# Optimization experiments

Measured on AMD Instinct MI355X. Metric: run time of the kernel, lower is better.

Reference implementation:

```python
import jax, jax.numpy as jnp
import numpy as np

B, H, S, D = 4, 16, 2048, 64
SCALE = 8.0  # sqrt(D)
NEG = -1000000000.0


def setup_inputs() -> dict:
    key = jax.random.key(0)
    kq, kk, kv = jax.random.split(key, 3)
    q = jax.random.normal(kq, (B, H, S, D), dtype=jnp.float32)
    k = jax.random.normal(kk, (B, H, S, D), dtype=jnp.float32)
    v = jax.random.normal(kv, (B, H, S, D), dtype=jnp.float32)
    # causal mask: True means masked out (matches torch masked_fill)
    mask = jnp.triu(jnp.ones((S, S), dtype=bool), k=1)[None, None, :, :]
    mask = jnp.broadcast_to(mask, (B, 1, S, S))
    return {"q": q, "k": k, "v": v, "mask": mask}


def reference(q, k, v, mask):
    # score = q @ k^T / scale  -> [B,H,S,S]
    score = jnp.einsum("bhqd,bhkd->bhqk", q, k) / SCALE
    score = jnp.where(mask, NEG, score)
    probs = jax.nn.softmax(score, axis=-1)
    context = jnp.einsum("bhqk,bhkd->bhqd", probs, v)
    return context
```

## Files before the change

kernel.cpp:

```cpp
#include <hip/hip_runtime.h>

#define SQ 2048
#define DH 64
#define BK 64
#define NQT 32
#define NBH 64
#define M0 8.0f

#define WS_BYTES ((size_t)2 * NBH * SQ * DH * 2)

typedef float f32x4 __attribute__((ext_vector_type(4)));
typedef __bf16 bf16x8 __attribute__((ext_vector_type(8)));
typedef _Float16 f16x4 __attribute__((ext_vector_type(4)));
typedef _Float16 f16x8 __attribute__((ext_vector_type(8)));
typedef __fp16 fp16x2 __attribute__((ext_vector_type(2)));
typedef unsigned short u16x8 __attribute__((ext_vector_type(8)));
typedef unsigned int u32x4 __attribute__((ext_vector_type(4)));

#define WAIT_VM(N) asm volatile("s_waitcnt vmcnt(" #N ")" ::: "memory")

static __device__ __forceinline__ unsigned int pkbf(float a, float b) {
#if __has_builtin(__builtin_amdgcn_cvt_pk_bf16_f32)
  typedef __bf16 bf16x2 __attribute__((ext_vector_type(2)));
  bf16x2 r = __builtin_amdgcn_cvt_pk_bf16_f32(a, b);
  return __builtin_bit_cast(unsigned int, r);
#else
  unsigned int ua = __builtin_bit_cast(unsigned int, a);
  unsigned int ub = __builtin_bit_cast(unsigned int, b);
  ua += 0x7fffu + ((ua >> 16) & 1u);
  ub += 0x7fffu + ((ub >> 16) & 1u);
  return (ua >> 16) | (ub & 0xffff0000u);
#endif
}

static __device__ __forceinline__ unsigned int pkf16(float a, float b) {
  fp16x2 r = __builtin_amdgcn_cvt_pkrtz(a, b);
  return __builtin_bit_cast(unsigned int, r);
}

static __device__ __forceinline__ f32x4 mfma_qk(u16x8 a, u16x8 b, f32x4 c) {
  return __builtin_amdgcn_mfma_f32_16x16x32_bf16(
      __builtin_bit_cast(bf16x8, a), __builtin_bit_cast(bf16x8, b), c, 0, 0, 0);
}

static __device__ __forceinline__ f32x4 mfma_pv(f16x4 a, f16x4 b, f32x4 c) {
  return __builtin_amdgcn_mfma_f32_16x16x16f16(a, b, c, 0, 0, 0);
}

static __device__ __forceinline__ f32x4 mfma_pv32(f16x8 a, f16x8 b, f32x4 c) {
  return __builtin_amdgcn_mfma_f32_16x16x32_f16(a, b, c, 0, 0, 0);
}

static __device__ __forceinline__ void ld16(unsigned short* l, const unsigned short* g) {
  __builtin_amdgcn_global_load_lds(
      (const __attribute__((address_space(1))) unsigned int*)(const void*)g,
      (__attribute__((address_space(3))) unsigned int*)(void*)l, 16, 0, 0);
}

static __device__ __forceinline__ void store_tile(float* wb, float* dst,
                                                  const f32x4* o, int lane,
                                                  int l15, int quad) {
#pragma unroll
  for (int dt = 0; dt < 4; ++dt) {
    const int colw = dt * 16 + quad * 4;
    *(f32x4*)&wb[l15 * 64 + (colw ^ ((l15 & 3) * 16))] = o[dt];
  }
  __builtin_amdgcn_wave_barrier();
#pragma unroll
  for (int j = 0; j < 4; ++j) {
    const int row = j * 4 + (lane >> 4);
    const int colw = (lane & 15) * 4;
    f32x4 v = *(const f32x4*)&wb[row * 64 + (colw ^ ((row & 3) * 16))];
    *(f32x4*)&dst[row * 64 + colw] = v;
  }
}

__global__ __launch_bounds__(256) void prep(const float* __restrict__ K,
                                            const float* __restrict__ V,
                                            unsigned short* __restrict__ Kf,
                                            unsigned short* __restrict__ Vf) {
  const int bh = (int)blockIdx.x >> 5;
  const int st = (int)blockIdx.x & 31;
  const int tid = threadIdx.x;
  __shared__ __align__(16) unsigned short T[DH * 64];
  {
    const int kvb = (tid >> 4) * 4, vdb = (tid & 15) * 4;
    const float* vp = V + ((size_t)bh * SQ + st * 64 + kvb) * DH + vdb;
    f32x4 r0 = *(const f32x4*)vp, r1 = *(const f32x4*)(vp + DH),
          r2 = *(const f32x4*)(vp + 2 * DH), r3 = *(const f32x4*)(vp + 3 * DH);
    const int uu = kvb >> 3, h = (kvb >> 2) & 1;
#pragma unroll
    for (int i = 0; i < 4; ++i) {
      const int d = vdb + i;
      uint2 w = {pkf16(r0[i], r1[i]), pkf16(r2[i], r3[i])};
      *(uint2*)&T[d * 64 + ((uu ^ (d & 7)) * 8) + h * 4] = w;
    }
  }
  {
    const size_t kin = ((size_t)bh * SQ + st * 64) * DH;
    unsigned short* kfo = Kf + (size_t)bh * SQ * DH + (size_t)st * 64 * DH;
#pragma unroll
    for (int e = 0; e < 2; ++e) {
      const int L = tid * 2 + e;
      const int l15 = L & 15, quad = (L >> 4) & 3, c = (L >> 6) & 1, nt = (L >> 7) & 3;
      const int krow = (nt >> 1) * 32 + ((l15 >> 2) & 3) * 8 + (nt & 1) * 4 + (l15 & 3);
      const float* kp = K + kin + (size_t)krow * DH + (c * 4 + quad) * 8;
      f32x4 x = *(const f32x4*)kp, y = *(const f32x4*)(kp + 4);
      u32x4 w = {pkbf(x[0], x[1]), pkbf(x[2], x[3]), pkbf(y[0], y[1]), pkbf(y[2], y[3])};
      *(u32x4*)&kfo[L * 8] = w;
    }
  }
  __syncthreads();
  {
    unsigned short* vfo = Vf + (size_t)bh * SQ * DH + (size_t)st * 64 * DH;
#pragma unroll
    for (int e = 0; e < 2; ++e) {
      const int L = tid * 2 + e;
      const int l15 = L & 15, quad = (L >> 4) & 3, dt = (L >> 6) & 3, n2 = (L >> 8) & 1;
      const int d = dt * 16 + l15, uu = n2 * 4 + quad;
      u16x8 val = *(const u16x8*)&T[d * 64 + ((uu ^ (d & 7)) * 8)];
      *(u16x8*)&vfo[L * 8] = val;
    }
  }
}

__global__ __launch_bounds__(512, 4) void fa_main(
    const float* __restrict__ Q, const unsigned short* __restrict__ Kf,
    const unsigned short* __restrict__ Vf, float* __restrict__ O) {
  const int lin = (int)blockIdx.x;
  const int xcd = lin & 7, u = lin >> 3;
  const int hh = u & 7;
  const int p = (int)((0x32104567u >> ((u >> 3) * 4)) & 15u);
  const int bh = hh * 8 + xcd;
  const int tend = 4 * p + 3;

  const int tid = threadIdx.x;
  const int wv = tid >> 6;
  const int lane = tid & 63;
  const int l15 = lane & 15;
  const int quad = lane >> 4;

  __shared__ __align__(16) unsigned short SS[4][8192];

  const size_t hq = (size_t)bh * (SQ * DH);
  const unsigned short* KfH = Kf + (size_t)bh * SQ * DH;
  const unsigned short* VfH = Vf + (size_t)bh * SQ * DH;

  const int qbase = p * 256 + wv * 32;
  const int dtw = 4 * p + (wv >> 1);
  const int qo = (wv & 1) * 32;

  u16x8 qf[2][2];
  {
    const float scq = 0.125f * 1.4426950408889634f;
#pragma unroll
    for (int f = 0; f < 2; ++f) {
      const float* qp = Q + hq + (size_t)(qbase + 16 * f + l15) * DH + quad * 8;
#pragma unroll
      for (int c = 0; c < 2; ++c) {
        f32x4 x = *(const f32x4*)(qp + c * 32);
        f32x4 y = *(const f32x4*)(qp + c * 32 + 4);
        u32x4 w = {pkbf(x[0] * scq, x[1] * scq), pkbf(x[2] * scq, x[3] * scq),
                   pkbf(y[0] * scq, y[1] * scq), pkbf(y[2] * scq, y[3] * scq)};
        qf[f][c] = __builtin_bit_cast(u16x8, w);
      }
    }
  }

  f32x4 o0[4], o1[4], la0, la1;
#pragma unroll
  for (int dt = 0; dt < 4; ++dt) {
    o0[dt] = (f32x4){0.f, 0.f, 0.f, 0.f};
    o1[dt] = (f32x4){0.f, 0.f, 0.f, 0.f};
  }
  la0 = (f32x4){0.f, 0.f, 0.f, 0.f};
  la1 = (f32x4){0.f, 0.f, 0.f, 0.f};
  const f16x8 ones8 = {(_Float16)1.f, (_Float16)1.f, (_Float16)1.f, (_Float16)1.f,
                       (_Float16)1.f, (_Float16)1.f, (_Float16)1.f, (_Float16)1.f};

  auto stage = [&](unsigned short* W, int t) {
#pragma unroll
    for (int j = 0; j < 2; ++j) {
      const int off = wv * 1024 + j * 512 + lane * 8;
      const unsigned short* src = (off < 4096)
                                      ? &KfH[(size_t)t * 4096 + off]
                                      : &VfH[(size_t)t * 4096 + (off - 4096)];
      ld16(&W[off], src);
    }
  };

  auto attend = [&](const unsigned short* B, bool diag) {
    const unsigned short* Ks = B;
    const unsigned short* Vs = B + 4096;
    f32x4 s0[4], s1[4];
#pragma unroll
    for (int nt = 0; nt < 4; ++nt) {
      f32x4 a0 = {-M0, -M0, -M0, -M0}, a1 = {-M0, -M0, -M0, -M0};
#pragma unroll
      for (int c = 0; c < 2; ++c) {
        u16x8 kf = *(const u16x8*)&Ks[(nt * 2 + c) * 512 + lane * 8];
        a0 = mfma_qk(kf, qf[0][c], a0);
        a1 = mfma_qk(kf, qf[1][c], a1);
      }
      s0[nt] = a0;
      s1[nt] = a1;
    }
    if (diag) {
#pragma unroll
      for (int nt = 0; nt < 4; ++nt)
#pragma unroll
        for (int r = 0; r < 4; ++r) {
          const int kvl = (nt >> 1) * 32 + quad * 8 + (nt & 1) * 4 + r;
          if (kvl > qo + l15) s0[nt][r] = -1e30f;
          if (kvl > qo + 16 + l15) s1[nt][r] = -1e30f;
        }
    }
    f16x8 pf0[2], pf1[2];
#pragma unroll
    for (int n2 = 0; n2 < 2; ++n2) {
      f32x4 pe0, po0, pe1, po1;
#pragma unroll
      for (int r = 0; r < 4; ++r) {
        pe0[r] = __builtin_amdgcn_exp2f(s0[2 * n2][r]);
        po0[r] = __builtin_amdgcn_exp2f(s0[2 * n2 + 1][r]);
        pe1[r] = __builtin_amdgcn_exp2f(s1[2 * n2][r]);
        po1[r] = __builtin_amdgcn_exp2f(s1[2 * n2 + 1][r]);
      }
      u32x4 w0 = {pkf16(pe0[0], pe0[1]), pkf16(pe0[2], pe0[3]),
                  pkf16(po0[0], po0[1]), pkf16(po0[2], po0[3])};
      u32x4 w1 = {pkf16(pe1[0], pe1[1]), pkf16(pe1[2], pe1[3]),
                  pkf16(po1[0], po1[1]), pkf16(po1[2], po1[3])};
      pf0[n2] = __builtin_bit_cast(f16x8, w0);
      pf1[n2] = __builtin_bit_cast(f16x8, w1);
    }
#pragma unroll
    for (int n2 = 0; n2 < 2; ++n2) {
      la0 = mfma_pv32(ones8, pf0[n2], la0);
      la1 = mfma_pv32(ones8, pf1[n2], la1);
    }
#pragma unroll
    for (int dt = 0; dt < 4; ++dt) {
#pragma unroll
      for (int n2 = 0; n2 < 2; ++n2) {
        f16x8 vf = *(const f16x8*)&Vs[(n2 * 4 + dt) * 512 + lane * 8];
        o0[dt] = mfma_pv32(vf, pf0[n2], o0[dt]);
        o1[dt] = mfma_pv32(vf, pf1[n2], o1[dt]);
      }
    }
  };

  stage(SS[0], 0);
  stage(SS[1], 1);
  stage(SS[2], 2);
  WAIT_VM(4);
  __builtin_amdgcn_s_barrier();
  __builtin_amdgcn_sched_barrier(0);

  for (int t = 0; t <= tend; ++t) {
    if (t + 3 <= tend) stage(SS[(t + 3) & 3], t + 3);
    if (t <= dtw) attend(SS[t & 3], t == dtw);
    const int rem = tend - t;
    if (rem >= 3) {
      WAIT_VM(4);
    } else if (rem == 2) {
      WAIT_VM(2);
    } else {
      WAIT_VM(0);
    }
    __builtin_amdgcn_s_barrier();
    __builtin_amdgcn_sched_barrier(0);
  }

  float* wb = (float*)SS + wv * 1024;
  {
    const float inv = 1.0f / la0[0];
    f32x4 on[4];
#pragma unroll
    for (int dt = 0; dt < 4; ++dt) on[dt] = o0[dt] * inv;
    store_tile(wb, O + hq + (size_t)(qbase)*DH, on, lane, l15, quad);
  }
  {
    const float inv = 1.0f / la1[0];
    f32x4 on[4];
#pragma unroll
    for (int dt = 0; dt < 4; ++dt) on[dt] = o1[dt] * inv;
    store_tile(wb, O + hq + (size_t)(qbase + 16) * DH, on, lane, l15, quad);
  }
}

__global__ __launch_bounds__(256, 4) void fa_full(
    const float* __restrict__ Q, const float* __restrict__ K,
    const float* __restrict__ V, float* __restrict__ O) {
  const int lin = (int)blockIdx.x;
  const int xcd = lin & 7;
  const int u = lin >> 3;
  const int hh = u & 7;
  const int p = u >> 3;
  const int bh = hh * 8 + xcd;
  const int tid = threadIdx.x;
  const int wv = tid >> 6;
  const int lane = tid & 63;
  const int l15 = lane & 15;
  const int quad = lane >> 4;
  __shared__ __align__(16) unsigned short SMEM[2][2 * BK * DH];
  const size_t hbase = (size_t)bh * (SQ * DH);
  const int krr = tid >> 3, kcc = (tid & 7) * 8;
  const int kvb = (tid >> 4) * 4, vdb = (tid & 15) * 4;
#pragma unroll
  for (int ph = 0; ph < 2; ++ph) {
    const int qt = ph ? (NQT - 1 - p) : p;
    const int wq0 = qt * 64 + wv * 16;
    u16x8 qf[2];
    {
      const float scq = 0.125f * 1.4426950408889634f;
      const float* qp = Q + hbase + (size_t)(wq0 + l15) * DH + quad * 8;
#pragma unroll
      for (int c = 0; c < 2; ++c) {
        f32x4 x = *(const f32x4*)(qp + c * 32);
        f32x4 y = *(const f32x4*)(qp + c * 32 + 4);
        u32x4 w = {pkbf(x[0] * scq, x[1] * scq), pkbf(x[2] * scq, x[3] * scq),
                   pkbf(y[0] * scq, y[1] * scq), pkbf(y[2] * scq, y[3] * scq)};
        qf[c] = __builtin_bit_cast(u16x8, w);
      }
    }
    f32x4 o[4];
#pragma unroll
    for (int dt = 0; dt < 4; ++dt) o[dt] = (f32x4){0.f, 0.f, 0.f, 0.f};
    float l = 0.f;
    f32x4 ka[2][2], va[4];
    {
      const float* kp = K + hbase + (size_t)krr * DH + kcc;
      ka[0][0] = *(const f32x4*)kp;             ka[0][1] = *(const f32x4*)(kp + 4);
      ka[1][0] = *(const f32x4*)(kp + 32 * DH); ka[1][1] = *(const f32x4*)(kp + 32 * DH + 4);
      const float* vp = V + hbase + (size_t)kvb * DH + vdb;
      va[0] = *(const f32x4*)vp;            va[1] = *(const f32x4*)(vp + DH);
      va[2] = *(const f32x4*)(vp + 2 * DH); va[3] = *(const f32x4*)(vp + 3 * DH);
    }
    __syncthreads();
    {
      unsigned short* Ksn = SMEM[0];
      unsigned short* Vsn = SMEM[0] + BK * DH;
#pragma unroll
      for (int h = 0; h < 2; ++h) {
        const int rr = h * 32 + krr;
        u32x4 w = {pkbf(ka[h][0][0], ka[h][0][1]), pkbf(ka[h][0][2], ka[h][0][3]),
                   pkbf(ka[h][1][0], ka[h][1][1]), pkbf(ka[h][1][2], ka[h][1][3])};
        *(u32x4*)&Ksn[rr * DH + (kcc ^ ((rr & 7) * 8))] = w;
      }
#pragma unroll
      for (int i = 0; i < 4; ++i) {
        const int d = vdb + i;
        uint2 w = {pkf16(va[0][i], va[1][i]), pkf16(va[2][i], va[3][i])};
        *(uint2*)&Vsn[d * BK + (kvb ^ ((d & 15) * 4))] = w;
      }
    }
    __syncthreads();
    for (int t = 0; t <= qt; ++t) {
      const unsigned short* Ks = SMEM[t & 1];
      const unsigned short* Vs = SMEM[t & 1] + BK * DH;
      if (t < qt) {
        const int kb2 = (t + 1) * BK;
        const float* kp = K + hbase + (size_t)(kb2 + krr) * DH + kcc;
        ka[0][0] = *(const f32x4*)kp;             ka[0][1] = *(const f32x4*)(kp + 4);
        ka[1][0] = *(const f32x4*)(kp + 32 * DH); ka[1][1] = *(const f32x4*)(kp + 32 * DH + 4);
        const float* vp = V + hbase + (size_t)(kb2 + kvb) * DH + vdb;
        va[0] = *(const f32x4*)vp;            va[1] = *(const f32x4*)(vp + DH);
        va[2] = *(const f32x4*)(vp + 2 * DH); va[3] = *(const f32x4*)(vp + 3 * DH);
      }
      f32x4 s[4];
#pragma unroll
      for (int nt = 0; nt < 4; ++nt) {
        f32x4 acc = {-M0, -M0, -M0, -M0};
#pragma unroll
        for (int c = 0; c < 2; ++c) {
          const int row = nt * 16 + l15;
          u16x8 kf = *(const u16x8*)&Ks[row * DH + ((c * 32 + quad * 8) ^ ((l15 & 7) * 8))];
          acc = mfma_qk(kf, qf[c], acc);
        }
        s[nt] = acc;
      }
      if (t == qt) {
#pragma unroll
        for (int nt = 0; nt < 4; ++nt)
#pragma unroll
          for (int r = 0; r < 4; ++r)
            if (nt * 16 + quad * 4 + r > wv * 16 + l15) s[nt][r] = -1e30f;
      }
      f16x4 pf[4];
#pragma unroll
      for (int nt = 0; nt < 4; ++nt) {
        f32x4 pr;
#pragma unroll
        for (int r = 0; r < 4; ++r) { pr[r] = __builtin_amdgcn_exp2f(s[nt][r]); l += pr[r]; }
        uint2 w2 = {pkf16(pr[0], pr[1]), pkf16(pr[2], pr[3])};
        pf[nt] = __builtin_bit_cast(f16x4, w2);
      }
#pragma unroll
      for (int dt = 0; dt < 4; ++dt) {
        const int d = dt * 16 + l15;
#pragma unroll
        for (int nt = 0; nt < 4; ++nt) {
          f16x4 vf = *(const f16x4*)&Vs[d * BK + ((nt * 16 + quad * 4) ^ (l15 * 4))];
          o[dt] = mfma_pv(vf, pf[nt], o[dt]);
        }
      }
      if (t < qt) {
        unsigned short* Ksn = SMEM[(t + 1) & 1];
        unsigned short* Vsn = SMEM[(t + 1) & 1] + BK * DH;
#pragma unroll
        for (int h = 0; h < 2; ++h) {
          const int rr = h * 32 + krr;
          u32x4 w = {pkbf(ka[h][0][0], ka[h][0][1]), pkbf(ka[h][0][2], ka[h][0][3]),
                     pkbf(ka[h][1][0], ka[h][1][1]), pkbf(ka[h][1][2], ka[h][1][3])};
          *(u32x4*)&Ksn[rr * DH + (kcc ^ ((rr & 7) * 8))] = w;
        }
#pragma unroll
        for (int i = 0; i < 4; ++i) {
          const int d = vdb + i;
          uint2 w = {pkf16(va[0][i], va[1][i]), pkf16(va[2][i], va[3][i])};
          *(uint2*)&Vsn[d * BK + (kvb ^ ((d & 15) * 4))] = w;
        }
        __syncthreads();
      }
    }
    l += __shfl_xor(l, 16, 64);
    l += __shfl_xor(l, 32, 64);
    const float inv = 1.0f / l;
    f32x4 on[4];
#pragma unroll
    for (int dt = 0; dt < 4; ++dt) on[dt] = o[dt] * inv;
    float* wb = (float*)SMEM[(qt + 1) & 1] + wv * 1024;
    store_tile(wb, O + hbase + (size_t)wq0 * DH, on, lane, l15, quad);
  }
}

extern "C" void kernel_launch(void* const* d_in, const int* in_sizes, int n_in,
                              void* d_out, int out_size, void* d_ws, size_t ws_size,
                              hipStream_t stream) {
  const float* q = (const float*)d_in[0];
  const float* k = (const float*)d_in[1];
  const float* v = (const float*)d_in[2];
  float* o = (float*)d_out;
  if (ws_size >= WS_BYTES) {
    unsigned short* Kf = (unsigned short*)d_ws;
    unsigned short* Vf = Kf + (size_t)NBH * SQ * DH;
    prep<<<dim3(NBH * 32), 256, 0, stream>>>(k, v, Kf, Vf);
    fa_main<<<dim3(512), 512, 0, stream>>>(q, Kf, Vf, o);
  } else {
    fa_full<<<dim3(1024), 256, 0, stream>>>(q, k, v, o);
  }
}
```

Measured before the change: 204.0 us.

## Pair complementary causal query tiles per block to balance work in one launch

Each block now processes two query tiles, p and 7-p, back to back, so every block streams the same 36 key/value tiles and causal work is balanced. The grid is halved to 256 blocks and launch bounds drop to 2 waves per SIMD. The pipeline now stages two tiles per step and waits for all loads (vmcnt 0) before each barrier. Output stores go directly to global memory instead of through the LDS-staged store_tile. The risks are lower parallelism with only 256 blocks on a 256-CU device, a pipeline that drains fully every step, and less coalesced output writes.

New measurement: 211.2 us. 3.5% more time.

```diff
diff --git a/kernel.cpp b/kernel.cpp
--- a/kernel.cpp
+++ b/kernel.cpp
@@ -17,7 +17,7 @@
 typedef unsigned short u16x8 __attribute__((ext_vector_type(8)));
 typedef unsigned int u32x4 __attribute__((ext_vector_type(4)));
 
-#define WAIT_VM(N) asm volatile("s_waitcnt vmcnt(" #N ")" ::: "memory")
+#define WAIT_VM0() asm volatile("s_waitcnt vmcnt(0)" ::: "memory")
 
 static __device__ __forceinline__ unsigned int pkbf(float a, float b) {
 #if __has_builtin(__builtin_amdgcn_cvt_pk_bf16_f32)
@@ -124,15 +124,17 @@
   }
 }
 
-__global__ __launch_bounds__(512, 4) void fa_main(
+__global__ __launch_bounds__(512, 2) void fa_main(
     const float* __restrict__ Q, const unsigned short* __restrict__ Kf,
     const unsigned short* __restrict__ Vf, float* __restrict__ O) {
   const int lin = (int)blockIdx.x;
   const int xcd = lin & 7, u = lin >> 3;
   const int hh = u & 7;
-  const int p = (int)((0x32104567u >> ((u >> 3) * 4)) & 15u);
+  const int p = u >> 3;
   const int bh = hh * 8 + xcd;
-  const int tend = 4 * p + 3;
+
+  const int LA = 4 * p + 4;
+  const int NS = 36;
 
   const int tid = threadIdx.x;
   const int wv = tid >> 6;
@@ -146,16 +148,18 @@
   const unsigned short* KfH = Kf + (size_t)bh * SQ * DH;
   const unsigned short* VfH = Vf + (size_t)bh * SQ * DH;
 
-  const int qbase = p * 256 + wv * 32;
-  const int dtw = 4 * p + (wv >> 1);
   const int qo = (wv & 1) * 32;
+  const int qbA = p * 256 + wv * 32;
+  const int qbB = (7 - p) * 256 + wv * 32;
+  const int dtwA = 4 * p + (wv >> 1);
+  const int dtwB = 4 * (7 - p) + (wv >> 1);
 
   u16x8 qf[2][2];
-  {
+  auto loadQ = [&](int qb) {
     const float scq = 0.125f * 1.4426950408889634f;
 #pragma unroll
     for (int f = 0; f < 2; ++f) {
-      const float* qp = Q + hq + (size_t)(qbase + 16 * f + l15) * DH + quad * 8;
+      const float* qp = Q + hq + (size_t)(qb + 16 * f + l15) * DH + quad * 8;
 #pragma unroll
       for (int c = 0; c < 2; ++c) {
         f32x4 x = *(const f32x4*)(qp + c * 32);
@@ -165,16 +169,18 @@
         qf[f][c] = __builtin_bit_cast(u16x8, w);
       }
     }
-  }
+  };
 
   f32x4 o0[4], o1[4], la0, la1;
-#pragma unroll
-  for (int dt = 0; dt < 4; ++dt) {
-    o0[dt] = (f32x4){0.f, 0.f, 0.f, 0.f};
-    o1[dt] = (f32x4){0.f, 0.f, 0.f, 0.f};
-  }
-  la0 = (f32x4){0.f, 0.f, 0.f, 0.f};
-  la1 = (f32x4){0.f, 0.f, 0.f, 0.f};
+  auto zacc = [&]() {
+#pragma unroll
+    for (int dt = 0; dt < 4; ++dt) {
+      o0[dt] = (f32x4){0.f, 0.f, 0.f, 0.f};
+      o1[dt] = (f32x4){0.f, 0.f, 0.f, 0.f};
+    }
+    la0 = (f32x4){0.f, 0.f, 0.f, 0.f};
+    la1 = (f32x4){0.f, 0.f, 0.f, 0.f};
+  };
   const f16x8 ones8 = {(_Float16)1.f, (_Float16)1.f, (_Float16)1.f, (_Float16)1.f,
                        (_Float16)1.f, (_Float16)1.f, (_Float16)1.f, (_Float16)1.f};
 
@@ -249,43 +255,58 @@
     }
   };
 
-  stage(SS[0], 0);
-  stage(SS[1], 1);
-  stage(SS[2], 2);
-  WAIT_VM(4);
+  auto flush = [&](int qb) {
+    const float inv0 = 1.0f / la0[0];
+    const float inv1 = 1.0f / la1[0];
+#pragma unroll
+    for (int f = 0; f < 2; ++f) {
+      const f32x4* oo = f ? o1 : o0;
+      const float inv = f ? inv1 : inv0;
+      float* dst = O + hq + (size_t)(qb + f * 16 + l15) * DH + quad * 4;
+#pragma unroll
+      for (int dt = 0; dt < 4; ++dt) {
+        f32x4 v = oo[dt] * inv;
+        *(f32x4*)(dst + dt * 16) = v;
+      }
+    }
+  };
+
+  auto tof = [&](int j) { return j < LA ? j : j - LA; };
+  auto astep = [&](int j) {
+    if (j < LA) {
+      if (j <= dtwA) attend(SS[j & 3], j == dtwA);
+    } else {
+      const int t = j - LA;
+      if (t <= dtwB) attend(SS[j & 3], t == dtwB);
+    }
+  };
+
+  loadQ(qbA);
+  zacc();
+
+  stage(SS[0], tof(0));
+  stage(SS[1], tof(1));
+  WAIT_VM0();
   __builtin_amdgcn_s_barrier();
-  __builtin_amdgcn_sched_barrier(0);
-
-  for (int t = 0; t <= tend; ++t) {
-    if (t + 3 <= tend) stage(SS[(t + 3) & 3], t + 3);
-    if (t <= dtw) attend(SS[t & 3], t == dtw);
-    const int rem = tend - t;
-    if (rem >= 3) {
-      WAIT_VM(4);
-    } else if (rem == 2) {
-      WAIT_VM(2);
-    } else {
-      WAIT_VM(0);
-    }
+
+  for (int q = 0; q < 18; ++q) {
+    const int j0 = 2 * q, j1 = j0 + 1;
+    if (j0 + 2 < NS) {
+      stage(SS[(j0 + 2) & 3], tof(j0 + 2));
+      stage(SS[(j1 + 2) & 3], tof(j1 + 2));
+    }
+    astep(j0);
+    astep(j1);
+    if (j1 == LA - 1) {
+      flush(qbA);
+      loadQ(qbB);
+      zacc();
+    }
+    WAIT_VM0();
     __builtin_amdgcn_s_barrier();
-    __builtin_amdgcn_sched_barrier(0);
-  }
-
-  float* wb = (float*)SS + wv * 1024;
-  {
-    const float inv = 1.0f / la0[0];
-    f32x4 on[4];
-#pragma unroll
-    for (int dt = 0; dt < 4; ++dt) on[dt] = o0[dt] * inv;
-    store_tile(wb, O + hq + (size_t)(qbase)*DH, on, lane, l15, quad);
-  }
-  {
-    const float inv = 1.0f / la1[0];
-    f32x4 on[4];
-#pragma unroll
-    for (int dt = 0; dt < 4; ++dt) on[dt] = o1[dt] * inv;
-    store_tile(wb, O + hq + (size_t)(qbase + 16) * DH, on, lane, l15, quad);
-  }
+  }
+
+  flush(qbB);
 }
 
 __global__ __launch_bounds__(256, 4) void fa_full(
@@ -445,7 +466,7 @@
     unsigned short* Kf = (unsigned short*)d_ws;
     unsigned short* Vf = Kf + (size_t)NBH * SQ * DH;
     prep<<<dim3(NBH * 32), 256, 0, stream>>>(k, v, Kf, Vf);
-    fa_main<<<dim3(512), 512, 0, stream>>>(q, Kf, Vf, o);
+    fa_main<<<dim3(256), 512, 0, stream>>>(q, Kf, Vf, o);
   } else {
     fa_full<<<dim3(1024), 256, 0, stream>>>(q, k, v, o);
   }
```

## Give each wave an independent 64-row query tile with private K staging

Applied to the files above, without the earlier changes.

Restructures fa_main so each of 4 waves owns a full 64-row query tile, pairing light and heavy causal tiles for balance. Each wave stages its own K slices into private LDS and loads V straight into registers, so the per-iteration block barrier is gone. Four query fragments now share every K/V fragment, which raises register pressure and duplicates K/V global loads across waves. The output is written directly from registers instead of through an LDS transpose.

After: 215.9 us. 5.8% more time.

```diff
diff --git a/kernel.cpp b/kernel.cpp
--- a/kernel.cpp
+++ b/kernel.cpp
@@ -124,15 +124,13 @@
   }
 }
 
-__global__ __launch_bounds__(512, 4) void fa_main(
+__global__ __launch_bounds__(256, 2) void fa_main(
     const float* __restrict__ Q, const unsigned short* __restrict__ Kf,
     const unsigned short* __restrict__ Vf, float* __restrict__ O) {
   const int lin = (int)blockIdx.x;
   const int xcd = lin & 7, u = lin >> 3;
-  const int hh = u & 7;
-  const int p = (int)((0x32104567u >> ((u >> 3) * 4)) & 15u);
+  const int hh = u & 7, k = u >> 3;
   const int bh = hh * 8 + xcd;
-  const int tend = 4 * p + 3;
 
   const int tid = threadIdx.x;
   const int wv = tid >> 6;
@@ -140,22 +138,21 @@
   const int l15 = lane & 15;
   const int quad = lane >> 4;
 
-  __shared__ __align__(16) unsigned short SS[4][8192];
+  const int sg = (wv < 2) ? (2 * k + wv) : (31 - 2 * k - (wv & 1));
+  const int qb = sg * 64;
+
+  __shared__ __align__(16) unsigned short KS[4][2][4096];
 
   const size_t hq = (size_t)bh * (SQ * DH);
   const unsigned short* KfH = Kf + (size_t)bh * SQ * DH;
   const unsigned short* VfH = Vf + (size_t)bh * SQ * DH;
 
-  const int qbase = p * 256 + wv * 32;
-  const int dtw = 4 * p + (wv >> 1);
-  const int qo = (wv & 1) * 32;
-
-  u16x8 qf[2][2];
+  u16x8 qf[4][2];
   {
     const float scq = 0.125f * 1.4426950408889634f;
 #pragma unroll
-    for (int f = 0; f < 2; ++f) {
-      const float* qp = Q + hq + (size_t)(qbase + 16 * f + l15) * DH + quad * 8;
+    for (int f = 0; f < 4; ++f) {
+      const float* qp = Q + hq + (size_t)(qb + 16 * f + l15) * DH + quad * 8;
 #pragma unroll
       for (int c = 0; c < 2; ++c) {
         f32x4 x = *(const f32x4*)(qp + c * 32);
@@ -167,124 +164,107 @@
     }
   }
 
-  f32x4 o0[4], o1[4], la0, la1;
-#pragma unroll
-  for (int dt = 0; dt < 4; ++dt) {
-    o0[dt] = (f32x4){0.f, 0.f, 0.f, 0.f};
-    o1[dt] = (f32x4){0.f, 0.f, 0.f, 0.f};
-  }
-  la0 = (f32x4){0.f, 0.f, 0.f, 0.f};
-  la1 = (f32x4){0.f, 0.f, 0.f, 0.f};
+  f32x4 o[4][4], la[4];
+#pragma unroll
+  for (int f = 0; f < 4; ++f) {
+    la[f] = (f32x4){0.f, 0.f, 0.f, 0.f};
+#pragma unroll
+    for (int dt = 0; dt < 4; ++dt) o[f][dt] = (f32x4){0.f, 0.f, 0.f, 0.f};
+  }
   const f16x8 ones8 = {(_Float16)1.f, (_Float16)1.f, (_Float16)1.f, (_Float16)1.f,
                        (_Float16)1.f, (_Float16)1.f, (_Float16)1.f, (_Float16)1.f};
 
-  auto stage = [&](unsigned short* W, int t) {
-#pragma unroll
-    for (int j = 0; j < 2; ++j) {
-      const int off = wv * 1024 + j * 512 + lane * 8;
-      const unsigned short* src = (off < 4096)
-                                      ? &KfH[(size_t)t * 4096 + off]
-                                      : &VfH[(size_t)t * 4096 + (off - 4096)];
-      ld16(&W[off], src);
-    }
+  f16x8 vb[8];
+  auto loadV = [&](int t) {
+#pragma unroll
+    for (int i = 0; i < 8; ++i)
+      vb[i] = *(const f16x8*)&VfH[(size_t)t * 4096 + i * 512 + lane * 8];
   };
-
-  auto attend = [&](const unsigned short* B, bool diag) {
-    const unsigned short* Ks = B;
-    const unsigned short* Vs = B + 4096;
-    f32x4 s0[4], s1[4];
-#pragma unroll
-    for (int nt = 0; nt < 4; ++nt) {
-      f32x4 a0 = {-M0, -M0, -M0, -M0}, a1 = {-M0, -M0, -M0, -M0};
-#pragma unroll
-      for (int c = 0; c < 2; ++c) {
-        u16x8 kf = *(const u16x8*)&Ks[(nt * 2 + c) * 512 + lane * 8];
-        a0 = mfma_qk(kf, qf[0][c], a0);
-        a1 = mfma_qk(kf, qf[1][c], a1);
-      }
-      s0[nt] = a0;
-      s1[nt] = a1;
-    }
-    if (diag) {
-#pragma unroll
-      for (int nt = 0; nt < 4; ++nt)
+  auto stageK = [&](int slot, int t) {
+#pragma unroll
+    for (int i = 0; i < 8; ++i)
+      ld16(&KS[wv][slot][i * 512 + lane * 8],
+           &KfH[(size_t)t * 4096 + i * 512 + lane * 8]);
+  };
+
+  auto attend = [&](const unsigned short* Ks, bool diag) {
+#pragma unroll
+    for (int n2 = 0; n2 < 2; ++n2) {
+      f32x4 s[4][2];
+#pragma unroll
+      for (int f = 0; f < 4; ++f) {
+        s[f][0] = (f32x4){-M0, -M0, -M0, -M0};
+        s[f][1] = (f32x4){-M0, -M0, -M0, -M0};
+      }
+#pragma unroll
+      for (int ntl = 0; ntl < 2; ++ntl)
+#pragma unroll
+        for (int c = 0; c < 2; ++c) {
+          u16x8 kf = *(const u16x8*)&Ks[((n2 * 2 + ntl) * 2 + c) * 512 + lane * 8];
+#pragma unroll
+          for (int f = 0; f < 4; ++f) s[f][ntl] = mfma_qk(kf, qf[f][c], s[f][ntl]);
+        }
+      if (diag) {
+#pragma unroll
+        for (int f = 0; f < 4; ++f)
+#pragma unroll
+          for (int ntl = 0; ntl < 2; ++ntl)
+#pragma unroll
+            for (int r = 0; r < 4; ++r) {
+              const int kvl = n2 * 32 + quad * 8 + ntl * 4 + r;
+              if (kvl > 16 * f + l15) s[f][ntl][r] = -1e30f;
+            }
+      }
+      f16x8 pf[4];
+#pragma unroll
+      for (int f = 0; f < 4; ++f) {
+        f32x4 pe, po;
 #pragma unroll
         for (int r = 0; r < 4; ++r) {
-          const int kvl = (nt >> 1) * 32 + quad * 8 + (nt & 1) * 4 + r;
-          if (kvl > qo + l15) s0[nt][r] = -1e30f;
-          if (kvl > qo + 16 + l15) s1[nt][r] = -1e30f;
-        }
-    }
-    f16x8 pf0[2], pf1[2];
-#pragma unroll
-    for (int n2 = 0; n2 < 2; ++n2) {
-      f32x4 pe0, po0, pe1, po1;
-#pragma unroll
-      for (int r = 0; r < 4; ++r) {
-        pe0[r] = __builtin_amdgcn_exp2f(s0[2 * n2][r]);
-        po0[r] = __builtin_amdgcn_exp2f(s0[2 * n2 + 1][r]);
-        pe1[r] = __builtin_amdgcn_exp2f(s1[2 * n2][r]);
-        po1[r] = __builtin_amdgcn_exp2f(s1[2 * n2 + 1][r]);
-      }
-      u32x4 w0 = {pkf16(pe0[0], pe0[1]), pkf16(pe0[2], pe0[3]),
-                  pkf16(po0[0], po0[1]), pkf16(po0[2], po0[3])};
-      u32x4 w1 = {pkf16(pe1[0], pe1[1]), pkf16(pe1[2], pe1[3]),
-                  pkf16(po1[0], po1[1]), pkf16(po1[2], po1[3])};
-      pf0[n2] = __builtin_bit_cast(f16x8, w0);
-      pf1[n2] = __builtin_bit_cast(f16x8, w1);
-    }
-#pragma unroll
-    for (int n2 = 0; n2 < 2; ++n2) {
-      la0 = mfma_pv32(ones8, pf0[n2], la0);
-      la1 = mfma_pv32(ones8, pf1[n2], la1);
-    }
-#pragma unroll
-    for (int dt = 0; dt < 4; ++dt) {
-#pragma unroll
-      for (int n2 = 0; n2 < 2; ++n2) {
-        f16x8 vf = *(const f16x8*)&Vs[(n2 * 4 + dt) * 512 + lane * 8];
-        o0[dt] = mfma_pv32(vf, pf0[n2], o0[dt]);
-        o1[dt] = mfma_pv32(vf, pf1[n2], o1[dt]);
+          pe[r] = __builtin_amdgcn_exp2f(s[f][0][r]);
+          po[r] = __builtin_amdgcn_exp2f(s[f][1][r]);
+        }
+        u32x4 w = {pkf16(pe[0], pe[1]), pkf16(pe[2], pe[3]),
+                   pkf16(po[0], po[1]), pkf16(po[2], po[3])};
+        pf[f] = __builtin_bit_cast(f16x8, w);
+      }
+#pragma unroll
+      for (int f = 0; f < 4; ++f) la[f] = mfma_pv32(ones8, pf[f], la[f]);
+#pragma unroll
+      for (int dt = 0; dt < 4; ++dt) {
+        const f16x8 vf = vb[n2 * 4 + dt];
+#pragma unroll
+        for (int f = 0; f < 4; ++f) o[f][dt] = mfma_pv32(vf, pf[f], o[f][dt]);
       }
     }
   };
 
-  stage(SS[0], 0);
-  stage(SS[1], 1);
-  stage(SS[2], 2);
-  WAIT_VM(4);
-  __builtin_amdgcn_s_barrier();
-  __builtin_amdgcn_sched_barrier(0);
-
-  for (int t = 0; t <= tend; ++t) {
-    if (t + 3 <= tend) stage(SS[(t + 3) & 3], t + 3);
-    if (t <= dtw) attend(SS[t & 3], t == dtw);
-    const int rem = tend - t;
-    if (rem >= 3) {
-      WAIT_VM(4);
-    } else if (rem == 2) {
-      WAIT_VM(2);
+  stageK(0, 0);
+  loadV(0);
+  if (sg >= 1) stageK(1, 1);
+
+  for (int t = 0; t <= sg; ++t) {
+    if (t < sg) {
+      WAIT_VM(8);
     } else {
       WAIT_VM(0);
     }
-    __builtin_amdgcn_s_barrier();
     __builtin_amdgcn_sched_barrier(0);
-  }
-
-  float* wb = (float*)SS + wv * 1024;
-  {
-    const float inv = 1.0f / la0[0];
-    f32x4 on[4];
-#pragma unroll
-    for (int dt = 0; dt < 4; ++dt) on[dt] = o0[dt] * inv;
-    store_tile(wb, O + hq + (size_t)(qbase)*DH, on, lane, l15, quad);
-  }
-  {
-    const float inv = 1.0f / la1[0];
-    f32x4 on[4];
-#pragma unroll
-    for (int dt = 0; dt < 4; ++dt) on[dt] = o1[dt] * inv;
-    store_tile(wb, O + hq + (size_t)(qbase + 16) * DH, on, lane, l15, quad);
+    attend(&KS[wv][t & 1][0], t == sg);
+    __builtin_amdgcn_sched_barrier(0);
+    if (t + 1 <= sg) loadV(t + 1);
+    if (t + 2 <= sg) stageK(t & 1, t + 2);
+  }
+
+#pragma unroll
+  for (int f = 0; f < 4; ++f) {
+    const float inv = 1.0f / la[f][0];
+    float* dst = O + hq + (size_t)(qb + f * 16 + l15) * DH + quad * 4;
+#pragma unroll
+    for (int dt = 0; dt < 4; ++dt) {
+      f32x4 v = o[f][dt] * inv;
+      *(f32x4*)(dst + dt * 16) = v;
+    }
   }
 }
 
@@ -445,7 +425,7 @@
     unsigned short* Kf = (unsigned short*)d_ws;
     unsigned short* Vf = Kf + (size_t)NBH * SQ * DH;
     prep<<<dim3(NBH * 32), 256, 0, stream>>>(k, v, Kf, Vf);
-    fa_main<<<dim3(512), 512, 0, stream>>>(q, Kf, Vf, o);
+    fa_main<<<dim3(512), 256, 0, stream>>>(q, Kf, Vf, o);
   } else {
     fa_full<<<dim3(1024), 256, 0, stream>>>(q, k, v, o);
   }
```

## Restructure fa_main into per-wave independent strips with paired causal load balancing

Applied to the files above, without the earlier changes.

Rewrites the main attention kernel so each of 4 waves in a 256-thread block processes its own 32-row query strip independently, with private double-buffered K tiles in LDS and V fragments loaded straight from global memory into registers. Each wave handles strip p0 and its mirror 63-p0, which evens out causal work. The block-wide barriers used for shared K/V staging are removed. In exchange, waves in a block no longer share K/V loads, so global and L2 traffic per useful FLOP goes up. Output is now written directly from registers instead of through an LDS transpose.

After: 210.5 us. 3.2% more time.

```diff
diff --git a/kernel.cpp b/kernel.cpp
--- a/kernel.cpp
+++ b/kernel.cpp
@@ -124,15 +124,13 @@
   }
 }
 
-__global__ __launch_bounds__(512, 4) void fa_main(
+__global__ __launch_bounds__(256, 2) void fa_main(
     const float* __restrict__ Q, const unsigned short* __restrict__ Kf,
     const unsigned short* __restrict__ Vf, float* __restrict__ O) {
   const int lin = (int)blockIdx.x;
   const int xcd = lin & 7, u = lin >> 3;
-  const int hh = u & 7;
-  const int p = (int)((0x32104567u >> ((u >> 3) * 4)) & 15u);
+  const int hh = u & 7, j = u >> 3;
   const int bh = hh * 8 + xcd;
-  const int tend = 4 * p + 3;
 
   const int tid = threadIdx.x;
   const int wv = tid >> 6;
@@ -140,152 +138,156 @@
   const int l15 = lane & 15;
   const int quad = lane >> 4;
 
-  __shared__ __align__(16) unsigned short SS[4][8192];
+  const int p0 = j * 4 + wv;
+
+  __shared__ __align__(16) unsigned short KS[4][2][4096];
 
   const size_t hq = (size_t)bh * (SQ * DH);
   const unsigned short* KfH = Kf + (size_t)bh * SQ * DH;
   const unsigned short* VfH = Vf + (size_t)bh * SQ * DH;
 
-  const int qbase = p * 256 + wv * 32;
-  const int dtw = 4 * p + (wv >> 1);
-  const int qo = (wv & 1) * 32;
-
-  u16x8 qf[2][2];
-  {
-    const float scq = 0.125f * 1.4426950408889634f;
-#pragma unroll
-    for (int f = 0; f < 2; ++f) {
-      const float* qp = Q + hq + (size_t)(qbase + 16 * f + l15) * DH + quad * 8;
-#pragma unroll
-      for (int c = 0; c < 2; ++c) {
-        f32x4 x = *(const f32x4*)(qp + c * 32);
-        f32x4 y = *(const f32x4*)(qp + c * 32 + 4);
-        u32x4 w = {pkbf(x[0] * scq, x[1] * scq), pkbf(x[2] * scq, x[3] * scq),
-                   pkbf(y[0] * scq, y[1] * scq), pkbf(y[2] * scq, y[3] * scq)};
-        qf[f][c] = __builtin_bit_cast(u16x8, w);
-      }
-    }
-  }
-
-  f32x4 o0[4], o1[4], la0, la1;
-#pragma unroll
-  for (int dt = 0; dt < 4; ++dt) {
-    o0[dt] = (f32x4){0.f, 0.f, 0.f, 0.f};
-    o1[dt] = (f32x4){0.f, 0.f, 0.f, 0.f};
-  }
-  la0 = (f32x4){0.f, 0.f, 0.f, 0.f};
-  la1 = (f32x4){0.f, 0.f, 0.f, 0.f};
   const f16x8 ones8 = {(_Float16)1.f, (_Float16)1.f, (_Float16)1.f, (_Float16)1.f,
                        (_Float16)1.f, (_Float16)1.f, (_Float16)1.f, (_Float16)1.f};
 
-  auto stage = [&](unsigned short* W, int t) {
-#pragma unroll
-    for (int j = 0; j < 2; ++j) {
-      const int off = wv * 1024 + j * 512 + lane * 8;
-      const unsigned short* src = (off < 4096)
-                                      ? &KfH[(size_t)t * 4096 + off]
-                                      : &VfH[(size_t)t * 4096 + (off - 4096)];
-      ld16(&W[off], src);
-    }
+  auto stageK = [&](int slot, int t) {
+#pragma unroll
+    for (int i = 0; i < 8; ++i)
+      ld16(&KS[wv][slot][i * 512 + lane * 8],
+           &KfH[(size_t)t * 4096 + i * 512 + lane * 8]);
   };
 
-  auto attend = [&](const unsigned short* B, bool diag) {
-    const unsigned short* Ks = B;
-    const unsigned short* Vs = B + 4096;
-    f32x4 s0[4], s1[4];
-#pragma unroll
-    for (int nt = 0; nt < 4; ++nt) {
-      f32x4 a0 = {-M0, -M0, -M0, -M0}, a1 = {-M0, -M0, -M0, -M0};
-#pragma unroll
-      for (int c = 0; c < 2; ++c) {
-        u16x8 kf = *(const u16x8*)&Ks[(nt * 2 + c) * 512 + lane * 8];
-        a0 = mfma_qk(kf, qf[0][c], a0);
-        a1 = mfma_qk(kf, qf[1][c], a1);
-      }
-      s0[nt] = a0;
-      s1[nt] = a1;
-    }
-    if (diag) {
-#pragma unroll
-      for (int nt = 0; nt < 4; ++nt)
+  auto run = [&](int s) {
+    const int sg = s >> 1;
+    const int qb = s * 32;
+    const int qo = (s & 1) * 32;
+
+    u16x8 qf[2][2];
+    {
+      const float scq = 0.125f * 1.4426950408889634f;
+#pragma unroll
+      for (int f = 0; f < 2; ++f) {
+        const float* qp = Q + hq + (size_t)(qb + 16 * f + l15) * DH + quad * 8;
+#pragma unroll
+        for (int c = 0; c < 2; ++c) {
+          f32x4 x = *(const f32x4*)(qp + c * 32);
+          f32x4 y = *(const f32x4*)(qp + c * 32 + 4);
+          u32x4 w = {pkbf(x[0] * scq, x[1] * scq), pkbf(x[2] * scq, x[3] * scq),
+                     pkbf(y[0] * scq, y[1] * scq), pkbf(y[2] * scq, y[3] * scq)};
+          qf[f][c] = __builtin_bit_cast(u16x8, w);
+        }
+      }
+    }
+
+    f32x4 o0[4], o1[4], la0, la1;
+#pragma unroll
+    for (int dt = 0; dt < 4; ++dt) {
+      o0[dt] = (f32x4){0.f, 0.f, 0.f, 0.f};
+      o1[dt] = (f32x4){0.f, 0.f, 0.f, 0.f};
+    }
+    la0 = (f32x4){0.f, 0.f, 0.f, 0.f};
+    la1 = (f32x4){0.f, 0.f, 0.f, 0.f};
+
+    f16x8 vb[8];
+    auto loadV = [&](int t) {
+#pragma unroll
+      for (int i = 0; i < 8; ++i)
+        vb[i] = *(const f16x8*)&VfH[(size_t)t * 4096 + i * 512 + lane * 8];
+    };
+
+    auto attend = [&](const unsigned short* Ks, bool diag) {
+      f32x4 s0[4], s1[4];
+#pragma unroll
+      for (int nt = 0; nt < 4; ++nt) {
+        f32x4 a0 = {-M0, -M0, -M0, -M0}, a1 = {-M0, -M0, -M0, -M0};
+#pragma unroll
+        for (int c = 0; c < 2; ++c) {
+          u16x8 kf = *(const u16x8*)&Ks[(nt * 2 + c) * 512 + lane * 8];
+          a0 = mfma_qk(kf, qf[0][c], a0);
+          a1 = mfma_qk(kf, qf[1][c], a1);
+        }
+        s0[nt] = a0;
+        s1[nt] = a1;
+      }
+      if (diag) {
+#pragma unroll
+        for (int nt = 0; nt < 4; ++nt)
+#pragma unroll
+          for (int r = 0; r < 4; ++r) {
+            const int kvl = (nt >> 1) * 32 + quad * 8 + (nt & 1) * 4 + r;
+            if (kvl > qo + l15) s0[nt][r] = -1e30f;
+            if (kvl > qo + 16 + l15) s1[nt][r] = -1e30f;
+          }
+      }
+      f16x8 pf0[2], pf1[2];
+#pragma unroll
+      for (int n2 = 0; n2 < 2; ++n2) {
+        f32x4 pe0, po0, pe1, po1;
 #pragma unroll
         for (int r = 0; r < 4; ++r) {
-          const int kvl = (nt >> 1) * 32 + quad * 8 + (nt & 1) * 4 + r;
-          if (kvl > qo + l15) s0[nt][r] = -1e30f;
-          if (kvl > qo + 16 + l15) s1[nt][r] = -1e30f;
-        }
-    }
-    f16x8 pf0[2], pf1[2];
-#pragma unroll
-    for (int n2 = 0; n2 < 2; ++n2) {
-      f32x4 pe0, po0, pe1, po1;
-#pragma unroll
-      for (int r = 0; r < 4; ++r) {
-        pe0[r] = __builtin_amdgcn_exp2f(s0[2 * n2][r]);
-        po0[r] = __builtin_amdgcn_exp2f(s0[2 * n2 + 1][r]);
-        pe1[r] = __builtin_amdgcn_exp2f(s1[2 * n2][r]);
-        po1[r] = __builtin_amdgcn_exp2f(s1[2 * n2 + 1][r]);
-      }
-      u32x4 w0 = {pkf16(pe0[0], pe0[1]), pkf16(pe0[2], pe0[3]),
-                  pkf16(po0[0], po0[1]), pkf16(po0[2], po0[3])};
-      u32x4 w1 = {pkf16(pe1[0], pe1[1]), pkf16(pe1[2], pe1[3]),
-                  pkf16(po1[0], po1[1]), pkf16(po1[2], po1[3])};
-      pf0[n2] = __builtin_bit_cast(f16x8, w0);
-      pf1[n2] = __builtin_bit_cast(f16x8, w1);
-    }
-#pragma unroll
-    for (int n2 = 0; n2 < 2; ++n2) {
-      la0 = mfma_pv32(ones8, pf0[n2], la0);
-      la1 = mfma_pv32(ones8, pf1[n2], la1);
-    }
-#pragma unroll
-    for (int dt = 0; dt < 4; ++dt) {
+          pe0[r] = __builtin_amdgcn_exp2f(s0[2 * n2][r]);
+          po0[r] = __builtin_amdgcn_exp2f(s0[2 * n2 + 1][r]);
+          pe1[r] = __builtin_amdgcn_exp2f(s1[2 * n2][r]);
+          po1[r] = __builtin_amdgcn_exp2f(s1[2 * n2 + 1][r]);
+        }
+        u32x4 w0 = {pkf16(pe0[0], pe0[1]), pkf16(pe0[2], pe0[3]),
+                    pkf16(po0[0], po0[1]), pkf16(po0[2], po0[3])};
+        u32x4 w1 = {pkf16(pe1[0], pe1[1]), pkf16(pe1[2], pe1[3]),
+                    pkf16(po1[0], po1[1]), pkf16(po1[2], po1[3])};
+        pf0[n2] = __builtin_bit_cast(f16x8, w0);
+        pf1[n2] = __builtin_bit_cast(f16x8, w1);
+      }
 #pragma unroll
       for (int n2 = 0; n2 < 2; ++n2) {
-        f16x8 vf = *(const f16x8*)&Vs[(n2 * 4 + dt) * 512 + lane * 8];
-        o0[dt] = mfma_pv32(vf, pf0[n2], o0[dt]);
-        o1[dt] = mfma_pv32(vf, pf1[n2], o1[dt]);
+        la0 = mfma_pv32(ones8, pf0[n2], la0);
+        la1 = mfma_pv32(ones8, pf1[n2], la1);
+      }
+#pragma unroll
+      for (int dt = 0; dt < 4; ++dt) {
+#pragma unroll
+        for (int n2 = 0; n2 < 2; ++n2) {
+          const f16x8 vf = vb[n2 * 4 + dt];
+          o0[dt] = mfma_pv32(vf, pf0[n2], o0[dt]);
+          o1[dt] = mfma_pv32(vf, pf1[n2], o1[dt]);
+        }
+      }
+    };
+
+    stageK(0, 0);
+    loadV(0);
+    if (sg >= 1) stageK(1, 1);
+
+    for (int t = 0; t <= sg; ++t) {
+      if (t < sg) {
+        WAIT_VM(8);
+      } else {
+        WAIT_VM(0);
+      }
+      __builtin_amdgcn_sched_barrier(0);
+      attend(&KS[wv][t & 1][0], t == sg);
+      __builtin_amdgcn_sched_barrier(0);
+      if (t + 1 <= sg) loadV(t + 1);
+      if (t + 2 <= sg) stageK(t & 1, t + 2);
+    }
+
+    {
+      const float inv0 = 1.0f / la0[0];
+      const float inv1 = 1.0f / la1[0];
+#pragma unroll
+      for (int f = 0; f < 2; ++f) {
+        const f32x4* oo = f ? o1 : o0;
+        const float inv = f ? inv1 : inv0;
+        float* dst = O + hq + (size_t)(qb + f * 16 + l15) * DH + quad * 4;
+#pragma unroll
+        for (int dt = 0; dt < 4; ++dt) {
+          f32x4 v = oo[dt] * inv;
+          *(f32x4*)(dst + dt * 16) = v;
+        }
       }
     }
   };
 
-  stage(SS[0], 0);
-  stage(SS[1], 1);
-  stage(SS[2], 2);
-  WAIT_VM(4);
-  __builtin_amdgcn_s_barrier();
-  __builtin_amdgcn_sched_barrier(0);
-
-  for (int t = 0; t <= tend; ++t) {
-    if (t + 3 <= tend) stage(SS[(t + 3) & 3], t + 3);
-    if (t <= dtw) attend(SS[t & 3], t == dtw);
-    const int rem = tend - t;
-    if (rem >= 3) {
-      WAIT_VM(4);
-    } else if (rem == 2) {
-      WAIT_VM(2);
-    } else {
-      WAIT_VM(0);
-    }
-    __builtin_amdgcn_s_barrier();
-    __builtin_amdgcn_sched_barrier(0);
-  }
-
-  float* wb = (float*)SS + wv * 1024;
-  {
-    const float inv = 1.0f / la0[0];
-    f32x4 on[4];
-#pragma unroll
-    for (int dt = 0; dt < 4; ++dt) on[dt] = o0[dt] * inv;
-    store_tile(wb, O + hq + (size_t)(qbase)*DH, on, lane, l15, quad);
-  }
-  {
-    const float inv = 1.0f / la1[0];
-    f32x4 on[4];
-#pragma unroll
-    for (int dt = 0; dt < 4; ++dt) on[dt] = o1[dt] * inv;
-    store_tile(wb, O + hq + (size_t)(qbase + 16) * DH, on, lane, l15, quad);
-  }
+  run(p0);
+  run(63 - p0);
 }
 
 __global__ __launch_bounds__(256, 4) void fa_full(
@@ -445,7 +447,7 @@
     unsigned short* Kf = (unsigned short*)d_ws;
     unsigned short* Vf = Kf + (size_t)NBH * SQ * DH;
     prep<<<dim3(NBH * 32), 256, 0, stream>>>(k, v, Kf, Vf);
-    fa_main<<<dim3(512), 512, 0, stream>>>(q, Kf, Vf, o);
+    fa_main<<<dim3(512), 256, 0, stream>>>(q, Kf, Vf, o);
   } else {
     fa_full<<<dim3(1024), 256, 0, stream>>>(q, k, v, o);
   }
```
